# Performance work log

Hardware: AMD Instinct MI355X
Metric: run time of the kernel (lower is better)

## Reference

```python
import jax, jax.numpy as jnp
import numpy as np

ROI = (8, 8)          # local window (kh, kw)
H = 768
W = 768
C = ROI[0] * ROI[1]   # 64 channels == prod(roi), required by the local conv
N_LAYERS = 4          # n_decoder_layers
LN_EPS = 1e-6         # flax.linen.LayerNorm default


def setup_inputs() -> dict:
    key = jax.random.key(0)
    k0, k1, k2 = jax.random.split(key, 3)
    x = jax.random.normal(k0, (H, W, C), jnp.float32)  # post-FPN feature map
    Ws = jax.random.normal(k1, (N_LAYERS, C, C), jnp.float32) / np.float32(np.sqrt(C))
    bs = jnp.zeros((N_LAYERS, C), jnp.float32)
    ln_scale = jnp.ones((N_LAYERS, C), jnp.float32)
    ln_bias = jnp.zeros((N_LAYERS, C), jnp.float32)
    w_out = jax.random.normal(k2, (C, 1), jnp.float32) / np.float32(np.sqrt(C))
    b_out = jnp.zeros((1,), jnp.float32)
    return {"x": x, "Ws": Ws, "bs": bs, "ln_scale": ln_scale,
            "ln_bias": ln_bias, "w_out": w_out, "b_out": b_out}


def att(x, weights):
    # out[i,j,c] = sum_{di,dj} xpad[i+di, j+dj, c] * weights[i, j, di*kw+dj]
    # Equivalent to the original per-channel lax.scan over
    # conv_general_dilated_local (window ordering row-major, 'same' padding),
    # but batched over all C channels at once via shifted-slice accumulation
    # instead of materializing the (H, W, 64, C) patch tensor.
    kh, kw = ROI
    pt, pb = (kh - 1) // 2, kh - 1 - (kh - 1) // 2  # 'SAME' pad for even kernel: (3, 4)
    pl, pr = (kw - 1) // 2, kw - 1 - (kw - 1) // 2
    xpad = jnp.pad(x, ((pt, pb), (pl, pr), (0, 0)))

    def body(acc, k):
        di = k // kw
        dj = k % kw
        patch = jax.lax.dynamic_slice(xpad, (di, dj, 0), (H, W, C))
        return acc + patch * weights[:, :, k][:, :, None], None

    acc, _ = jax.lax.scan(body, jnp.zeros_like(x), jnp.arange(kh * kw))
    return acc


def layer_norm(x, scale, bias):
    mu = jnp.mean(x, axis=-1, keepdims=True)
    var = jnp.mean(jnp.square(x - mu), axis=-1, keepdims=True)
    return (x - mu) * jax.lax.rsqrt(var + LN_EPS) * scale + bias


def reference(x, Ws, bs, ln_scale, ln_bias, w_out, b_out):
    weights = jax.nn.sigmoid(x)            # spatially-varying local-conv weights
    x0 = att(x, weights)                   # (H, W, C)
    for i in range(N_LAYERS):              # MLP decoder stack
        x0 = jax.nn.relu(x0 @ Ws[i] + bs[i])
        x0 = layer_norm(x0, ln_scale[i], ln_bias[i])
    out = x0 @ w_out + b_out               # (H, W, 1)
    return (x0, out)
```

## Files before the change

kernel.cpp:

```cpp
#include <hip/hip_runtime.h>
#include <hip/hip_bf16.h>


#define HH 768
#define WW 768
#define HWPX (HH*WW)

typedef __attribute__((ext_vector_type(8))) short short8;
typedef __attribute__((ext_vector_type(8))) _Float16 half8;
typedef __attribute__((ext_vector_type(4))) float f32x4;
typedef __attribute__((ext_vector_type(16))) float f32x16;

union hcvt { _Float16 h; ushort u; };
__device__ __forceinline__ ushort f2h(float f) { hcvt c; c.h = (_Float16)f; return c.u; }
__device__ __forceinline__ float sigmoidf(float v) { return 1.f / (1.f + __expf(-v)); }

__device__ __forceinline__ int goff(int row, int g) {
  return (row << 8) + ((g ^ (row & 31)) << 3);
}
__device__ __forceinline__ int eoff(int row, int k) {
  return (row << 8) + (((k >> 3) ^ (row & 31)) << 3) + (k & 7);
}

__global__ __launch_bounds__(256)
void prep_wf(const float* __restrict__ Ws, const float* __restrict__ bs,
             const float* __restrict__ lns, const float* __restrict__ lnb,
             ushort* __restrict__ Wfg) {
  const int L = threadIdx.x >> 6, co = threadIdx.x & 63;
  float bias = bs[L * 64 + co];
  float colsum = 0.f;
  ushort* row = Wfg + (size_t)(L * 64 + co) * 80;
  for (int ci = 0; ci < 64; ++ci) {
    const float w = Ws[((L * 64 + ci) << 6) + co];
    const float sc = (L > 0) ? lns[(L - 1) * 64 + ci] : 1.f;
    const float wp = sc * w;
    if (L > 0) bias += lnb[(L - 1) * 64 + ci] * w;
    colsum += wp;
    row[ci] = f2h(wp);
  }
  row[64] = f2h(bias);
  row[65] = f2h(colsum);
  for (int q = 66; q < 80; ++q) row[q] = 0;
}

template<bool F16OUT>
__global__ __launch_bounds__(512, 4)
void att_k1(const float* __restrict__ x, void* __restrict__ attout) {
  __shared__ __align__(16) ushort Mb[64 * 256];
  __shared__ __align__(16) ushort Xb[64 * 256];
  __shared__ __align__(16) float  scr[4 * 4 * 64 * 4];
  const int tid = threadIdx.x;
  const int lane = tid & 63, w = tid >> 6;
  const int l15 = lane & 15;
  const int l31 = lane & 31, lh = lane >> 5;
  const int ot = w & 3;
  const int pb = ot >> 1, cb2 = ot & 1;
  const int kh = w >> 2;

  {
    const short8 z8 = {0,0,0,0,0,0,0,0};
    #pragma unroll
    for (int i = 0; i < 4; ++i)
      *reinterpret_cast<short8*>(&Mb[(tid + i * 512) * 8]) = z8;
  }

  const int b = blockIdx.x;
  const int tbase = (b & 7) * 1152 + (b >> 3) * 18;
  const int p  = (w & 3) * 16 + l15;
  const int pr = p >> 3, pc = p & 7;
  const int cb = ((kh << 2) + (lane >> 4 & 3)) << 3;
  const int kr0 = pr + (cb >> 3);

  float4 cv[2];
  float Rv[2][8];
  float Lv[2][8];
  short8 rs[2];

  auto issue_loads = [&](int ti, int tj, bool fresh, bool fast) {
    {
      const float* cp = x + ((size_t)((ti + pr) * WW + (tj + pc)) << 6) + cb;
      cv[0] = *reinterpret_cast<const float4*>(cp);
      cv[1] = *reinterpret_cast<const float4*>(cp + 4);
    }
    #pragma unroll
    for (int i = 0; i < 2; ++i) {
      const int r = w + 8 * i;
      if (r < 15) {
        if (fast) {
          const int gr = ti + r - 3;
          const float* rowp = x + ((size_t)(gr * WW + tj) << 6) + lane;
          #pragma unroll
          for (int s = 0; s < 8; ++s)
            Rv[i][s] = rowp[(5 + s) << 6];
          if (fresh) {
            #pragma unroll
            for (int s = 0; s < 8; ++s)
              Lv[i][s] = rowp[(s - 3) << 6];
          }
        } else {
          const int gr = min(max(ti + r - 3, 0), HH - 1);
          const float* rowp = x + ((size_t)gr * WW << 6) + lane;
          #pragma unroll
          for (int s = 0; s < 8; ++s) {
            const int gc = min(max(tj + 5 + s, 0), WW - 1);
            Rv[i][s] = rowp[(size_t)gc << 6];
          }
          if (fresh) {
            #pragma unroll
            for (int s = 0; s < 8; ++s) {
              const int gc = min(max(tj - 3 + s, 0), WW - 1);
              Lv[i][s] = rowp[(size_t)gc << 6];
            }
          }
        }
      }
    }
  };

  auto write_lds = [&](int ti, int tj, bool fresh, bool fast) {
    #pragma unroll
    for (int qd = 0; qd < 2; ++qd) {
      const float vs[4] = {cv[qd].x, cv[qd].y, cv[qd].z, cv[qd].w};
      #pragma unroll
      for (int j = 0; j < 4; ++j) {
        const int k = (kr0 << 4) + pc + qd * 4 + j;
        Mb[eoff(p, k)] = f2h(sigmoidf(vs[j]));
      }
    }
    #pragma unroll
    for (int i = 0; i < 2; ++i) {
      const int r = w + 8 * i;
      if (r < 15) {
        short8 left8, right8;
        if (fast) {
          if (fresh) {
            #pragma unroll
            for (int s = 0; s < 8; ++s) left8[s] = (short)f2h(Lv[i][s]);
          } else {
            left8 = rs[i];
          }
          #pragma unroll
          for (int s = 0; s < 8; ++s) right8[s] = (short)f2h(Rv[i][s]);
        } else {
          const int gr = ti + r - 3;
          const bool rok = (unsigned)gr < (unsigned)HH;
          if (fresh) {
            #pragma unroll
            for (int s = 0; s < 8; ++s) {
              const int j = tj - 3 + s;
              const bool ok = rok && ((unsigned)j < (unsigned)WW);
              left8[s] = (short)f2h(ok ? Lv[i][s] : 0.f);
            }
          } else {
            left8 = rs[i];
          }
          #pragma unroll
          for (int s = 0; s < 8; ++s) {
            const int j = tj + 5 + s;
            const bool ok = rok && ((unsigned)j < (unsigned)WW);
            right8[s] = (short)f2h(ok ? Rv[i][s] : 0.f);
          }
        }
        *reinterpret_cast<short8*>(&Xb[goff(lane, 2 * r)])     = left8;
        *reinterpret_cast<short8*>(&Xb[goff(lane, 2 * r + 1)]) = right8;
        rs[i] = right8;
      }
    }
  };

  f32x16 acc;
  int pti = 0, ptj = 0;

  auto store_acc = [&](int ti, int tj) {
    #pragma unroll
    for (int reg = 0; reg < 16; ++reg) {
      const float v = acc[reg];
      const int prow = (reg & 3) + 8 * (reg >> 2) + 4 * lh;
      const int p2 = pb * 32 + prow;
      const size_t gpx = (size_t)(ti + (p2 >> 3)) * WW + (tj + (p2 & 7));
      const int ch = cb2 * 32 + l31;
      if (F16OUT) ((ushort*)attout)[(gpx << 6) + ch] = f2h(v);
      else        ((float*)attout)[(gpx << 6) + ch] = v;
    }
  };

  auto tile_fast = [](int ti, int tj, bool fresh) {
    return (ti != 0) && (ti != HH - 8) && (tj != WW - 8) && (!fresh || tj != 0);
  };

  {
    const int ti0 = (tbase / 96) * 8, tj0 = (tbase % 96) * 8;
    issue_loads(ti0, tj0, true, tile_fast(ti0, tj0, true));
  }

  for (int t18 = 0; t18 < 18; ++t18) {
    const int tile = tbase + t18;
    const int ti = (tile / 96) * 8, tj = (tile % 96) * 8;
    const bool fresh = (t18 == 0) || (tj == 0);

    __syncthreads();
    if (kh == 0 && t18 > 0) {
      #pragma unroll
      for (int q = 0; q < 4; ++q) {
        const float4 pv = *reinterpret_cast<const float4*>(&scr[ot * 1024 + q * 256 + lane * 4]);
        acc[q * 4 + 0] += pv.x; acc[q * 4 + 1] += pv.y;
        acc[q * 4 + 2] += pv.z; acc[q * 4 + 3] += pv.w;
      }
    }
    write_lds(ti, tj, fresh, tile_fast(ti, tj, fresh));
    __syncthreads();
    if (kh == 0 && t18 > 0) store_acc(pti, ptj);
    if (t18 < 17) {
      const int nt = tile + 1;
      const int nti = (nt / 96) * 8, ntj = (nt % 96) * 8;
      const bool nfresh = (nt % 96) == 0;
      issue_loads(nti, ntj, nfresh, tile_fast(nti, ntj, nfresh));
    }

    acc = (f32x16){0,0,0,0,0,0,0,0,0,0,0,0,0,0,0,0};
    const int ks0 = kh ? 7 : 0, ks1 = kh ? 15 : 7;
    #pragma unroll 8
    for (int ks = ks0; ks < ks1; ++ks) {
      const int g = 2 * ks + lh;
      const half8 a  = *reinterpret_cast<const half8*>(&Mb[goff(pb * 32 + l31, g)]);
      const half8 bb = *reinterpret_cast<const half8*>(&Xb[goff(cb2 * 32 + l31, g)]);
      acc = __builtin_amdgcn_mfma_f32_32x32x16_f16(a, bb, acc, 0, 0, 0);
    }
    if (kh == 1) {
      #pragma unroll
      for (int q = 0; q < 4; ++q) {
        float4 pv;
        pv.x = acc[q * 4 + 0]; pv.y = acc[q * 4 + 1];
        pv.z = acc[q * 4 + 2]; pv.w = acc[q * 4 + 3];
        *reinterpret_cast<float4*>(&scr[ot * 1024 + q * 256 + lane * 4]) = pv;
      }
    }
    pti = ti; ptj = tj;
  }
  __syncthreads();
  if (kh == 0) {
    #pragma unroll
    for (int q = 0; q < 4; ++q) {
      const float4 pv = *reinterpret_cast<const float4*>(&scr[ot * 1024 + q * 256 + lane * 4]);
      acc[q * 4 + 0] += pv.x; acc[q * 4 + 1] += pv.y;
      acc[q * 4 + 2] += pv.z; acc[q * 4 + 3] += pv.w;
    }
    store_acc(pti, ptj);
  }
}

__device__ __forceinline__ float zsel(const f32x16& z0, const f32x16& z1, int nb, int idx) {
  return nb ? z1[idx] : z0[idx];
}

template<bool F16IN>
__global__ __launch_bounds__(512, 2)
void mlp_k2(const void* attv, const ushort* __restrict__ Wfg,
            const float* __restrict__ lns, const float* __restrict__ lnb,
            const float* __restrict__ w_out, const float* __restrict__ b_out,
            float* x0_out, float* __restrict__ out1) {
  __shared__ __align__(16) ushort wt[4 * 64 * 88];
  __shared__ __align__(16) ushort act[8][32 * 88];
  __shared__ __align__(16) ushort kpat[16];
  const int tid = threadIdx.x;
  const int lane = tid & 63, wid = tid >> 6;
  const int l31 = lane & 31, lh = lane >> 5;

  for (int idx = tid; idx < 4 * 64 * 10; idx += 512) {
    const int row = idx / 10, q = idx - row * 10;
    *reinterpret_cast<uint4*>(&wt[row * 88 + q * 8]) =
        *reinterpret_cast<const uint4*>(&Wfg[(size_t)row * 80 + q * 8]);
  }
  for (int idx = tid; idx < 256; idx += 512) {
    ushort* rp = &act[idx >> 5][(idx & 31) * 88];
    for (int q = 64; q < 88; ++q) rp[q] = 0;
    rp[64] = 0x3C00;
  }
  if (tid < 16) kpat[tid] = (tid == 0) ? (ushort)0x3C00 : (ushort)0;

  float sc3[2][4][4], lb3[2][4][4], wo3[2][4][4];
  #pragma unroll
  for (int nb = 0; nb < 2; ++nb)
    #pragma unroll
    for (int hi = 0; hi < 4; ++hi)
      #pragma unroll
      for (int j = 0; j < 4; ++j) {
        const int ch = nb * 32 + hi * 8 + lh * 4 + j;
        sc3[nb][hi][j] = lns[192 + ch];
        lb3[nb][hi][j] = lnb[192 + ch];
        wo3[nb][hi][j] = w_out[ch];
      }
  const float b0s = b_out[0];
  __syncthreads();

  ushort* const myact = act[wid];

  for (int it = 0; it < 9; ++it) {
    const int px = ((it * 256 + (int)blockIdx.x) * 8 + wid) * 32 + l31;

    half8 bfr[5];
    if (F16IN) {
      const ushort* ap = (const ushort*)attv + ((size_t)px << 6) + lh * 8;
      #pragma unroll
      for (int g = 0; g < 4; ++g)
        bfr[g] = *reinterpret_cast<const half8*>(ap + g * 16);
    } else {
      const float* ap = (const float*)attv + ((size_t)px << 6) + lh * 8;
      #pragma unroll
      for (int g = 0; g < 4; ++g) {
        const float4 fa = *reinterpret_cast<const float4*>(ap + g * 16);
        const float4 fb = *reinterpret_cast<const float4*>(ap + g * 16 + 4);
        half8 h;
        h[0]=(_Float16)fa.x; h[1]=(_Float16)fa.y; h[2]=(_Float16)fa.z; h[3]=(_Float16)fa.w;
        h[4]=(_Float16)fb.x; h[5]=(_Float16)fb.y; h[6]=(_Float16)fb.z; h[7]=(_Float16)fb.w;
        bfr[g] = h;
      }
    }
    bfr[4] = *reinterpret_cast<const half8*>(&kpat[lh * 8]);

    f32x16 z0, z1;
    float mu = 0.f, rstd = 1.f;
    #pragma unroll
    for (int L = 0; L < 4; ++L) {
      if (L > 0) {
        #pragma unroll
        for (int g = 0; g < 5; ++g)
          bfr[g] = *reinterpret_cast<const half8*>(&myact[l31 * 88 + g * 16 + lh * 8]);
      }
      z0 = (f32x16){0,0,0,0,0,0,0,0,0,0,0,0,0,0,0,0};
      z1 = (f32x16){0,0,0,0,0,0,0,0,0,0,0,0,0,0,0,0};
      #pragma unroll
      for (int g = 0; g < 5; ++g) {
        const half8 a0 = *reinterpret_cast<const half8*>(&wt[(L * 64      + l31) * 88 + g * 16 + lh * 8]);
        const half8 a1 = *reinterpret_cast<const half8*>(&wt[(L * 64 + 32 + l31) * 88 + g * 16 + lh * 8]);
        z0 = __builtin_amdgcn_mfma_f32_32x32x16_f16(a0, bfr[g], z0, 0, 0, 0);
        z1 = __builtin_amdgcn_mfma_f32_32x32x16_f16(a1, bfr[g], z1, 0, 0, 0);
      }
      float sp[4] = {0.f, 0.f, 0.f, 0.f}, qp[4] = {0.f, 0.f, 0.f, 0.f};
      #pragma unroll
      for (int r = 0; r < 16; ++r) {
        const float v0 = fmaxf(z0[r], 0.f); z0[r] = v0;
        const float v1 = fmaxf(z1[r], 0.f); z1[r] = v1;
        sp[r & 3] += v0 + v1;
        qp[r & 3] += v0 * v0 + v1 * v1;
      }
      float s = (sp[0] + sp[1]) + (sp[2] + sp[3]);
      float qq = (qp[0] + qp[1]) + (qp[2] + qp[3]);
      s  += __shfl_xor(s, 32, 64);
      qq += __shfl_xor(qq, 32, 64);
      mu = s * 0.015625f;
      const float var = qq * 0.015625f - mu * mu;
      rstd = rsqrtf(var + 1e-6f);
      if (L < 3) {
        #pragma unroll
        for (int nb = 0; nb < 2; ++nb)
          #pragma unroll
          for (int hi = 0; hi < 4; ++hi) {
            ushort4 pk;
            pk.x = f2h(rstd * zsel(z0, z1, nb, hi * 4 + 0));
            pk.y = f2h(rstd * zsel(z0, z1, nb, hi * 4 + 1));
            pk.z = f2h(rstd * zsel(z0, z1, nb, hi * 4 + 2));
            pk.w = f2h(rstd * zsel(z0, z1, nb, hi * 4 + 3));
            *reinterpret_cast<ushort4*>(&myact[l31 * 88 + nb * 32 + hi * 8 + lh * 4]) = pk;
          }
        if (lh == 0) myact[l31 * 88 + 65] = f2h(-(mu * rstd));
      }
    }

    const float t = mu * rstd;
    float part0 = 0.f, part1 = 0.f;
    #pragma unroll
    for (int nb = 0; nb < 2; ++nb)
      #pragma unroll
      for (int hi = 0; hi < 4; ++hi) {
        f32x4 yv;
        #pragma unroll
        for (int j = 0; j < 4; ++j) {
          const float v = zsel(z0, z1, nb, hi * 4 + j);
          const float y = v * (rstd * sc3[nb][hi][j]) + (lb3[nb][hi][j] - t * sc3[nb][hi][j]);
          yv[j] = y;
          if (j & 1) part1 += y * wo3[nb][hi][j];
          else       part0 += y * wo3[nb][hi][j];
        }
        *reinterpret_cast<f32x4*>(&x0_out[((size_t)px << 6) + nb * 32 + hi * 8 + lh * 4]) = yv;
      }
    float part = part0 + part1;
    part += __shfl_xor(part, 32, 64);
    if (lh == 0) out1[px] = part + b0s;
  }
}

extern "C" void kernel_launch(void* const* d_in, const int* in_sizes, int n_in,
                              void* d_out, int out_size, void* d_ws, size_t ws_size,
                              hipStream_t stream) {
  const float* x     = (const float*)d_in[0];
  const float* Ws    = (const float*)d_in[1];
  const float* bs    = (const float*)d_in[2];
  const float* lns   = (const float*)d_in[3];
  const float* lnbv  = (const float*)d_in[4];
  const float* w_out = (const float*)d_in[5];
  const float* b_out = (const float*)d_in[6];
  float* x0_out = (float*)d_out;
  float* out1   = x0_out + (size_t)HWPX * 64;

  const size_t attBytes = (size_t)HWPX * 64 * sizeof(ushort);
  if (ws_size >= attBytes + 65536) {
    ushort* atth = (ushort*)d_ws;
    ushort* Wfg  = (ushort*)((char*)d_ws + attBytes);
    prep_wf<<<1, 256, 0, stream>>>(Ws, bs, lns, lnbv, Wfg);
    att_k1<true><<<512, 512, 0, stream>>>(x, atth);
    mlp_k2<true><<<256, 512, 0, stream>>>(atth, Wfg, lns, lnbv,
                                          w_out, b_out, x0_out, out1);
  } else {
    ushort* Wfg = (ushort*)d_ws;
    prep_wf<<<1, 256, 0, stream>>>(Ws, bs, lns, lnbv, Wfg);
    att_k1<false><<<512, 512, 0, stream>>>(x, d_out);
    mlp_k2<false><<<256, 512, 0, stream>>>(d_out, Wfg, lns, lnbv,
                                           w_out, b_out, x0_out, out1);
  }
}
```

Measured before the change: 180.2 us.

## Read MLP weights from global cache instead of LDS and double grid size

The MLP kernel no longer stages the 4x64x88 fp16 weight matrix in shared memory. Each lane reads its weight fragments straight from global memory, which should be cache-resident, and this frees about 45KB of LDS per block so more blocks can be resident. The grid doubles from 256 to 512 blocks with a bounds-checked loop over 2304 chunks, which gives better load balance and a larger wave count. The attention store is restructured to compute addresses per row group, which simplifies index arithmetic. In exchange, weight loads now go through VMEM and cache latency inside the MFMA loop instead of LDS.

```diff
diff --git a/kernel.cpp b/kernel.cpp
--- a/kernel.cpp
+++ b/kernel.cpp
@@ -172,15 +172,19 @@
   int pti = 0, ptj = 0;
 
   auto store_acc = [&](int ti, int tj) {
-    #pragma unroll
-    for (int reg = 0; reg < 16; ++reg) {
-      const float v = acc[reg];
-      const int prow = (reg & 3) + 8 * (reg >> 2) + 4 * lh;
-      const int p2 = pb * 32 + prow;
-      const size_t gpx = (size_t)(ti + (p2 >> 3)) * WW + (tj + (p2 & 7));
-      const int ch = cb2 * 32 + l31;
-      if (F16OUT) ((ushort*)attout)[(gpx << 6) + ch] = f2h(v);
-      else        ((float*)attout)[(gpx << 6) + ch] = v;
+    const int ch = cb2 * 32 + l31;
+    #pragma unroll
+    for (int q = 0; q < 4; ++q) {
+      const size_t gpx0 = (size_t)(ti + 4 * pb + q) * WW + (tj + 4 * lh);
+      if (F16OUT) {
+        ushort* bp = (ushort*)attout + (gpx0 << 6) + ch;
+        #pragma unroll
+        for (int j = 0; j < 4; ++j) bp[j << 6] = f2h(acc[q * 4 + j]);
+      } else {
+        float* bp = (float*)attout + (gpx0 << 6) + ch;
+        #pragma unroll
+        for (int j = 0; j < 4; ++j) bp[j << 6] = acc[q * 4 + j];
+      }
     }
   };
 
@@ -259,18 +263,12 @@
             const float* __restrict__ lns, const float* __restrict__ lnb,
             const float* __restrict__ w_out, const float* __restrict__ b_out,
             float* x0_out, float* __restrict__ out1) {
-  __shared__ __align__(16) ushort wt[4 * 64 * 88];
   __shared__ __align__(16) ushort act[8][32 * 88];
   __shared__ __align__(16) ushort kpat[16];
   const int tid = threadIdx.x;
   const int lane = tid & 63, wid = tid >> 6;
   const int l31 = lane & 31, lh = lane >> 5;
 
-  for (int idx = tid; idx < 4 * 64 * 10; idx += 512) {
-    const int row = idx / 10, q = idx - row * 10;
-    *reinterpret_cast<uint4*>(&wt[row * 88 + q * 8]) =
-        *reinterpret_cast<const uint4*>(&Wfg[(size_t)row * 80 + q * 8]);
-  }
   for (int idx = tid; idx < 256; idx += 512) {
     ushort* rp = &act[idx >> 5][(idx & 31) * 88];
     for (int q = 64; q < 88; ++q) rp[q] = 0;
@@ -291,12 +289,15 @@
         wo3[nb][hi][j] = w_out[ch];
       }
   const float b0s = b_out[0];
+  const ushort* wr0 = Wfg + (size_t)l31 * 80 + lh * 8;
   __syncthreads();
 
   ushort* const myact = act[wid];
 
-  for (int it = 0; it < 9; ++it) {
-    const int px = ((it * 256 + (int)blockIdx.x) * 8 + wid) * 32 + l31;
+  for (int it = 0; it < 5; ++it) {
+    const int chunk = it * 512 + (int)blockIdx.x;
+    if (chunk >= 2304) break;
+    const int px = (chunk * 8 + wid) * 32 + l31;
 
     half8 bfr[5];
     if (F16IN) {
@@ -329,10 +330,11 @@
       }
       z0 = (f32x16){0,0,0,0,0,0,0,0,0,0,0,0,0,0,0,0};
       z1 = (f32x16){0,0,0,0,0,0,0,0,0,0,0,0,0,0,0,0};
+      const ushort* wL = wr0 + (size_t)(L * 64) * 80;
       #pragma unroll
       for (int g = 0; g < 5; ++g) {
-        const half8 a0 = *reinterpret_cast<const half8*>(&wt[(L * 64      + l31) * 88 + g * 16 + lh * 8]);
-        const half8 a1 = *reinterpret_cast<const half8*>(&wt[(L * 64 + 32 + l31) * 88 + g * 16 + lh * 8]);
+        const half8 a0 = *reinterpret_cast<const half8*>(wL + g * 16);
+        const half8 a1 = *reinterpret_cast<const half8*>(wL + (size_t)32 * 80 + g * 16);
         z0 = __builtin_amdgcn_mfma_f32_32x32x16_f16(a0, bfr[g], z0, 0, 0, 0);
         z1 = __builtin_amdgcn_mfma_f32_32x32x16_f16(a1, bfr[g], z1, 0, 0, 0);
       }
@@ -409,13 +411,13 @@
     ushort* Wfg  = (ushort*)((char*)d_ws + attBytes);
     prep_wf<<<1, 256, 0, stream>>>(Ws, bs, lns, lnbv, Wfg);
     att_k1<true><<<512, 512, 0, stream>>>(x, atth);
-    mlp_k2<true><<<256, 512, 0, stream>>>(atth, Wfg, lns, lnbv,
+    mlp_k2<true><<<512, 512, 0, stream>>>(atth, Wfg, lns, lnbv,
                                           w_out, b_out, x0_out, out1);
   } else {
     ushort* Wfg = (ushort*)d_ws;
     prep_wf<<<1, 256, 0, stream>>>(Ws, bs, lns, lnbv, Wfg);
     att_k1<false><<<512, 512, 0, stream>>>(x, d_out);
-    mlp_k2<false><<<256, 512, 0, stream>>>(d_out, Wfg, lns, lnbv,
+    mlp_k2<false><<<512, 512, 0, stream>>>(d_out, Wfg, lns, lnbv,
                                            w_out, b_out, x0_out, out1);
   }
 }
```

After: 203.8 us. 1.13x slower.

## Double-buffer LDS tiles in local-attention kernel and pack cross-wave partials as fp16

Applied to the files above, without the earlier changes.

Restructures the att_k1 tile loop to double-buffer the weight and patch tiles in LDS, so the next tile is written while the current one is consumed by MFMA. This cuts the loop from two barriers per tile to one, and global loads are now issued two tiles ahead. The split-K partial sums exchanged between wave groups are stored as fp16 in a double-buffered scratch array instead of fp32. The larger LDS footprint forces launch_bounds down to one block per CU minimum, which reduces occupancy, and the fp16 partials lose some precision.

```diff
diff --git a/kernel.cpp b/kernel.cpp
--- a/kernel.cpp
+++ b/kernel.cpp
@@ -13,6 +13,7 @@
 
 union hcvt { _Float16 h; ushort u; };
 __device__ __forceinline__ ushort f2h(float f) { hcvt c; c.h = (_Float16)f; return c.u; }
+__device__ __forceinline__ float h2f(ushort u) { hcvt c; c.u = u; return (float)c.h; }
 __device__ __forceinline__ float sigmoidf(float v) { return 1.f / (1.f + __expf(-v)); }
 
 __device__ __forceinline__ int goff(int row, int g) {
@@ -44,11 +45,11 @@
 }
 
 template<bool F16OUT>
-__global__ __launch_bounds__(512, 4)
+__global__ __launch_bounds__(512, 1)
 void att_k1(const float* __restrict__ x, void* __restrict__ attout) {
-  __shared__ __align__(16) ushort Mb[64 * 256];
-  __shared__ __align__(16) ushort Xb[64 * 256];
-  __shared__ __align__(16) float  scr[4 * 4 * 64 * 4];
+  __shared__ __align__(16) ushort Mb[2 * 64 * 256];
+  __shared__ __align__(16) ushort Xb[2 * 64 * 256];
+  __shared__ __align__(16) ushort scrh[2][4096];
   const int tid = threadIdx.x;
   const int lane = tid & 63, w = tid >> 6;
   const int l15 = lane & 15;
@@ -60,7 +61,7 @@
   {
     const short8 z8 = {0,0,0,0,0,0,0,0};
     #pragma unroll
-    for (int i = 0; i < 4; ++i)
+    for (int i = 0; i < 8; ++i)
       *reinterpret_cast<short8*>(&Mb[(tid + i * 512) * 8]) = z8;
   }
 
@@ -117,14 +118,16 @@
     }
   };
 
-  auto write_lds = [&](int ti, int tj, bool fresh, bool fast) {
+  auto write_lds = [&](int ti, int tj, bool fresh, bool fast, int buf) {
+    ushort* const Mbase = Mb + buf * 16384;
+    ushort* const Xbase = Xb + buf * 16384;
     #pragma unroll
     for (int qd = 0; qd < 2; ++qd) {
       const float vs[4] = {cv[qd].x, cv[qd].y, cv[qd].z, cv[qd].w};
       #pragma unroll
       for (int j = 0; j < 4; ++j) {
         const int k = (kr0 << 4) + pc + qd * 4 + j;
-        Mb[eoff(p, k)] = f2h(sigmoidf(vs[j]));
+        Mbase[eoff(p, k)] = f2h(sigmoidf(vs[j]));
       }
     }
     #pragma unroll
@@ -161,8 +164,8 @@
             right8[s] = (short)f2h(ok ? Rv[i][s] : 0.f);
           }
         }
-        *reinterpret_cast<short8*>(&Xb[goff(lane, 2 * r)])     = left8;
-        *reinterpret_cast<short8*>(&Xb[goff(lane, 2 * r + 1)]) = right8;
+        *reinterpret_cast<short8*>(&Xbase[goff(lane, 2 * r)])     = left8;
+        *reinterpret_cast<short8*>(&Xbase[goff(lane, 2 * r + 1)]) = right8;
         rs[i] = right8;
       }
     }
@@ -184,67 +187,81 @@
     }
   };
 
+  auto fold_scr = [&](int sb) {
+    #pragma unroll
+    for (int q = 0; q < 4; ++q) {
+      const ushort4 pk = *reinterpret_cast<const ushort4*>(&scrh[sb][ot * 1024 + q * 256 + lane * 4]);
+      acc[q * 4 + 0] += h2f(pk.x); acc[q * 4 + 1] += h2f(pk.y);
+      acc[q * 4 + 2] += h2f(pk.z); acc[q * 4 + 3] += h2f(pk.w);
+    }
+  };
+
   auto tile_fast = [](int ti, int tj, bool fresh) {
     return (ti != 0) && (ti != HH - 8) && (tj != WW - 8) && (!fresh || tj != 0);
   };
+  auto tcoord = [&](int t, int& ti, int& tj) {
+    const int tile = tbase + t;
+    ti = (tile / 96) * 8; tj = (tile % 96) * 8;
+  };
 
   {
-    const int ti0 = (tbase / 96) * 8, tj0 = (tbase % 96) * 8;
+    int ti0, tj0; tcoord(0, ti0, tj0);
     issue_loads(ti0, tj0, true, tile_fast(ti0, tj0, true));
-  }
-
-  for (int t18 = 0; t18 < 18; ++t18) {
-    const int tile = tbase + t18;
-    const int ti = (tile / 96) * 8, tj = (tile % 96) * 8;
-    const bool fresh = (t18 == 0) || (tj == 0);
-
     __syncthreads();
-    if (kh == 0 && t18 > 0) {
+    write_lds(ti0, tj0, true, tile_fast(ti0, tj0, true), 0);
+    int ti1, tj1; tcoord(1, ti1, tj1);
+    const bool f1 = (tj1 == 0);
+    issue_loads(ti1, tj1, f1, tile_fast(ti1, tj1, f1));
+    __syncthreads();
+  }
+
+  for (int t = 0; t < 18; ++t) {
+    const int cur = t & 1;
+    int ti, tj; tcoord(t, ti, tj);
+
+    if (kh == 0 && t > 0) {
+      fold_scr((t - 1) & 1);
+      store_acc(pti, ptj);
+    }
+    if (t < 17) {
+      int nti, ntj; tcoord(t + 1, nti, ntj);
+      const bool nf = (ntj == 0);
+      write_lds(nti, ntj, nf, tile_fast(nti, ntj, nf), cur ^ 1);
+    }
+    if (t < 16) {
+      int nti, ntj; tcoord(t + 2, nti, ntj);
+      const bool nf = (ntj == 0);
+      issue_loads(nti, ntj, nf, tile_fast(nti, ntj, nf));
+    }
+
+    acc = (f32x16){0,0,0,0,0,0,0,0,0,0,0,0,0,0,0,0};
+    {
+      const ushort* Mbase = Mb + cur * 16384;
+      const ushort* Xbase = Xb + cur * 16384;
+      const int arow = pb * 32 + l31, brow = cb2 * 32 + l31;
+      const int ks0 = kh ? 7 : 0, ks1 = kh ? 15 : 7;
+      #pragma unroll 8
+      for (int ks = ks0; ks < ks1; ++ks) {
+        const int g = 2 * ks + lh;
+        const half8 a  = *reinterpret_cast<const half8*>(&Mbase[goff(arow, g)]);
+        const half8 bb = *reinterpret_cast<const half8*>(&Xbase[goff(brow, g)]);
+        acc = __builtin_amdgcn_mfma_f32_32x32x16_f16(a, bb, acc, 0, 0, 0);
+      }
+    }
+    if (kh == 1) {
       #pragma unroll
       for (int q = 0; q < 4; ++q) {
-        const float4 pv = *reinterpret_cast<const float4*>(&scr[ot * 1024 + q * 256 + lane * 4]);
-        acc[q * 4 + 0] += pv.x; acc[q * 4 + 1] += pv.y;
-        acc[q * 4 + 2] += pv.z; acc[q * 4 + 3] += pv.w;
-      }
-    }
-    write_lds(ti, tj, fresh, tile_fast(ti, tj, fresh));
+        ushort4 pk;
+        pk.x = f2h(acc[q * 4 + 0]); pk.y = f2h(acc[q * 4 + 1]);
+        pk.z = f2h(acc[q * 4 + 2]); pk.w = f2h(acc[q * 4 + 3]);
+        *reinterpret_cast<ushort4*>(&scrh[t & 1][ot * 1024 + q * 256 + lane * 4]) = pk;
+      }
+    }
+    pti = ti; ptj = tj;
     __syncthreads();
-    if (kh == 0 && t18 > 0) store_acc(pti, ptj);
-    if (t18 < 17) {
-      const int nt = tile + 1;
-      const int nti = (nt / 96) * 8, ntj = (nt % 96) * 8;
-      const bool nfresh = (nt % 96) == 0;
-      issue_loads(nti, ntj, nfresh, tile_fast(nti, ntj, nfresh));
-    }
-
-    acc = (f32x16){0,0,0,0,0,0,0,0,0,0,0,0,0,0,0,0};
-    const int ks0 = kh ? 7 : 0, ks1 = kh ? 15 : 7;
-    #pragma unroll 8
-    for (int ks = ks0; ks < ks1; ++ks) {
-      const int g = 2 * ks + lh;
-      const half8 a  = *reinterpret_cast<const half8*>(&Mb[goff(pb * 32 + l31, g)]);
-      const half8 bb = *reinterpret_cast<const half8*>(&Xb[goff(cb2 * 32 + l31, g)]);
-      acc = __builtin_amdgcn_mfma_f32_32x32x16_f16(a, bb, acc, 0, 0, 0);
-    }
-    if (kh == 1) {
-      #pragma unroll
-      for (int q = 0; q < 4; ++q) {
-        float4 pv;
-        pv.x = acc[q * 4 + 0]; pv.y = acc[q * 4 + 1];
-        pv.z = acc[q * 4 + 2]; pv.w = acc[q * 4 + 3];
-        *reinterpret_cast<float4*>(&scr[ot * 1024 + q * 256 + lane * 4]) = pv;
-      }
-    }
-    pti = ti; ptj = tj;
-  }
-  __syncthreads();
+  }
   if (kh == 0) {
-    #pragma unroll
-    for (int q = 0; q < 4; ++q) {
-      const float4 pv = *reinterpret_cast<const float4*>(&scr[ot * 1024 + q * 256 + lane * 4]);
-      acc[q * 4 + 0] += pv.x; acc[q * 4 + 1] += pv.y;
-      acc[q * 4 + 2] += pv.z; acc[q * 4 + 3] += pv.w;
-    }
+    fold_scr(17 & 1);
     store_acc(pti, ptj);
   }
 }
```

New measurement: 214.3 us. +18.9%, slower.
